# Kernel optimization log

Measured on AMD Instinct MI355X. Metric: run time of the kernel, lower is better.

Reference implementation:

```python
import jax, jax.numpy as jnp
import numpy as np

DEPTH, DIM, HEADS, DIM_HEAD = 6, 1024, 16, 64
INNER = HEADS * DIM_HEAD  # 1024
DFF = 4 * DIM             # 4096
SCALE = DIM_HEAD ** -0.5


def setup_inputs() -> dict:
    key = jax.random.key(0)
    ks = jax.random.split(key, 12)
    def w(k, shape, fan_in):
        return jax.random.normal(k, shape, dtype=jnp.float32) * (fan_in ** -0.5)
    return {
        "x":     jax.random.normal(ks[0], (2, 2048, DIM), dtype=jnp.float32),
        "Wq":    w(ks[1], (DEPTH, DIM, INNER), DIM),
        "Wkv":   w(ks[2], (DEPTH, DIM, 2 * INNER), DIM),
        "Wo":    w(ks[3], (DEPTH, INNER, DIM), INNER),
        "bo":    jnp.zeros((DEPTH, DIM), dtype=jnp.float32),
        "ln1_g": jnp.ones((DEPTH, DIM), dtype=jnp.float32),
        "ln1_b": jnp.zeros((DEPTH, DIM), dtype=jnp.float32),
        "ln2_g": jnp.ones((DEPTH, DIM), dtype=jnp.float32),
        "ln2_b": jnp.zeros((DEPTH, DIM), dtype=jnp.float32),
        "W1":    w(ks[4], (DEPTH, DIM, DFF), DIM),
        "b1":    jnp.zeros((DEPTH, DFF), dtype=jnp.float32),
        "W2":    w(ks[5], (DEPTH, DFF, DIM), DFF),
        "b2":    jnp.zeros((DEPTH, DIM), dtype=jnp.float32),
    }


def _layernorm(x, g, b, eps=1e-5):
    mu = jnp.mean(x, axis=-1, keepdims=True)
    var = jnp.mean(jnp.square(x - mu), axis=-1, keepdims=True)
    return (x - mu) * jax.lax.rsqrt(var + eps) * g + b


def reference(x, Wq, Wkv, Wo, bo, ln1_g, ln1_b, ln2_g, ln2_b, W1, b1, W2, b2):
    b, n, _ = x.shape
    for l in range(DEPTH):
        # --- PreNorm self-attention ---
        h = _layernorm(x, ln1_g[l], ln1_b[l])
        q = h @ Wq[l]                       # [b, n, inner]
        kv = h @ Wkv[l]
        k, v = jnp.split(kv, 2, axis=-1)
        def heads(t):
            return t.reshape(b, n, HEADS, DIM_HEAD).transpose(0, 2, 1, 3)  # [b, h, n, d]
        q, k, v = heads(q), heads(k), heads(v)
        dots = jnp.einsum('bhid,bhjd->bhij', q, k) * SCALE
        attn = jax.nn.softmax(dots, axis=-1)
        out = jnp.einsum('bhij,bhjd->bhid', attn, v)
        out = out.transpose(0, 2, 1, 3).reshape(b, n, INNER)
        x = out @ Wo[l] + bo[l] + x
        # --- PreNorm feed-forward (exact GELU, matching torch nn.GELU default) ---
        h = _layernorm(x, ln2_g[l], ln2_b[l])
        h = jax.nn.gelu(h @ W1[l] + b1[l], approximate=False)
        x = h @ W2[l] + b2[l] + x
    return x
```

## Files before the change

### kernel.cpp

```cpp
#include <hip/hip_runtime.h>
#include <hip/hip_bf16.h>
#include <cstdint>
#include <cstddef>

#define DEPTH 6
#define DIM   1024
#define HEADS 16
#define DIMH  64
#define INNER 1024
#define DFF   4096
#define SEQ   2048
#define NTOK  4096

typedef __attribute__((ext_vector_type(8))) short bf16x8;
typedef __attribute__((ext_vector_type(4))) short bf16x4;
typedef __attribute__((ext_vector_type(4))) float f32x4;
typedef __hip_bfloat16 bf16;

#define CS 0.18033688011112042f
#define SMAX 24.0f

__device__ __forceinline__ void gld_lds16(const void* g, void* l) {
  __builtin_amdgcn_global_load_lds(
      (const __attribute__((address_space(1))) unsigned int*)g,
      (__attribute__((address_space(3))) unsigned int*)l,
      16, 0, 0);
}

__global__ __launch_bounds__(256) void transpose_convert(
    const float* __restrict__ in, bf16* __restrict__ out,
    int K, int N, int row0, int orows)
{
  __shared__ float tile[32][33];
  const int d  = blockIdx.z;
  const int n0 = blockIdx.x * 32, k0 = blockIdx.y * 32;
  const int c = threadIdx.x & 31, rb = threadIdx.x >> 5;
  const float* src = in + ((size_t)d * K + k0) * N + n0;
#pragma unroll
  for (int rr = 0; rr < 4; ++rr) {
    int r = rb + rr * 8;
    tile[r][c] = src[(size_t)r * N + c];
  }
  __syncthreads();
  bf16* dst = out + ((size_t)d * orows + row0 + n0) * K + k0;
#pragma unroll
  for (int rr = 0; rr < 4; ++rr) {
    int r = rb + rr * 8;
    dst[(size_t)r * K + c] = __float2bfloat16(tile[c][r]);
  }
}

__global__ __launch_bounds__(256) void ln_kernel(
    const float* __restrict__ x, const float* __restrict__ g,
    const float* __restrict__ b, bf16* __restrict__ h)
{
  const int row = blockIdx.x;
  const int tid = threadIdx.x;
  const float4 xv = *(const float4*)(x + (size_t)row * DIM + tid * 4);
  float s  = xv.x + xv.y + xv.z + xv.w;
  float s2 = xv.x * xv.x + xv.y * xv.y + xv.z * xv.z + xv.w * xv.w;
#pragma unroll
  for (int off = 1; off < 64; off <<= 1) {
    s  += __shfl_xor(s, off);
    s2 += __shfl_xor(s2, off);
  }
  __shared__ float red[8];
  const int wave = tid >> 6, lane = tid & 63;
  if (lane == 0) { red[wave * 2] = s; red[wave * 2 + 1] = s2; }
  __syncthreads();
  const float ts  = red[0] + red[2] + red[4] + red[6];
  const float ts2 = red[1] + red[3] + red[5] + red[7];
  const float mu  = ts * (1.0f / DIM);
  const float var = ts2 * (1.0f / DIM) - mu * mu;
  const float rstd = rsqrtf(var + 1e-5f);
  const float4 gv = *(const float4*)(g + tid * 4);
  const float4 bv = *(const float4*)(b + tid * 4);
  bf16 hv[4];
  hv[0] = __float2bfloat16((xv.x - mu) * rstd * gv.x + bv.x);
  hv[1] = __float2bfloat16((xv.y - mu) * rstd * gv.y + bv.y);
  hv[2] = __float2bfloat16((xv.z - mu) * rstd * gv.z + bv.z);
  hv[3] = __float2bfloat16((xv.w - mu) * rstd * gv.w + bv.w);
  *(uint2*)(h + (size_t)row * DIM + tid * 4) = *(uint2*)hv;
}

template<int EPI, bool SWZ, int BN>
__global__ __launch_bounds__(256) void gemm_t(
    const bf16* __restrict__ A, const bf16* __restrict__ Bt,
    int N, int K,
    const float* __restrict__ bias,
    float* __restrict__ outf, bf16* __restrict__ outb,
    bf16* __restrict__ outq, bf16* __restrict__ outk, bf16* __restrict__ outvt)
{
  constexpr int NW = BN / 32;
  __shared__ alignas(16) bf16 As[128 * 64];
  __shared__ alignas(16) bf16 Bs[BN * 64];
  const int tid  = threadIdx.x;
  const int lane = tid & 63;
  const int wave = tid >> 6;
  const int wr = wave >> 1, wc = wave & 1;

  int bx, by;
  if (SWZ) {
    const int gx   = (int)gridDim.x;
    const int nwg  = gx * (int)gridDim.y;
    const int wg   = blockIdx.x + blockIdx.y * gx;
    const int xcd  = wg & 7;
    const int slot = wg >> 3;
    const int id   = xcd * (nwg >> 3) + slot;
    by = id / gx;
    bx = id % gx;
  } else {
    bx = blockIdx.x; by = blockIdx.y;
  }
  const int m0 = by * 128, n0 = bx * BN;
  const int sr = tid >> 3, pc = tid & 7;
  const int wbase = (tid & ~63) << 4;

  f32x4 acc[4][NW];
#pragma unroll
  for (int m = 0; m < 4; ++m)
#pragma unroll
    for (int n = 0; n < NW; ++n) acc[m][n] = (f32x4){0.f, 0.f, 0.f, 0.f};

  for (int k0 = 0; k0 < K; k0 += 64) {
#pragma unroll
    for (int it = 0; it < 4; ++it) {
      const int r  = it * 32 + sr;
      const int lc = pc ^ (r & 7);
      gld_lds16(A + (size_t)(m0 + r) * K + k0 + lc * 8, (char*)As + it * 4096 + wbase);
    }
#pragma unroll
    for (int it = 0; it < NW; ++it) {
      const int r  = it * 32 + sr;
      const int lc = pc ^ (r & 7);
      gld_lds16(Bt + (size_t)(n0 + r) * K + k0 + lc * 8, (char*)Bs + it * 4096 + wbase);
    }
    __syncthreads();
#pragma unroll
    for (int kk = 0; kk < 2; ++kk) {
      const int cb = kk * 4 + (lane >> 4);
      bf16x8 af[4], bfr[NW];
#pragma unroll
      for (int m = 0; m < 4; ++m) {
        const int r = wr * 64 + m * 16 + (lane & 15);
        af[m] = *(const bf16x8*)((const char*)As + r * 128 + ((cb ^ (r & 7)) << 4));
      }
#pragma unroll
      for (int n = 0; n < NW; ++n) {
        const int r = wc * (BN / 2) + n * 16 + (lane & 15);
        bfr[n] = *(const bf16x8*)((const char*)Bs + r * 128 + ((cb ^ (r & 7)) << 4));
      }
#pragma unroll
      for (int m = 0; m < 4; ++m)
#pragma unroll
        for (int n = 0; n < NW; ++n)
          acc[m][n] = __builtin_amdgcn_mfma_f32_16x16x32_bf16(af[m], bfr[n], acc[m][n], 0, 0, 0);
    }
    __syncthreads();
  }

#pragma unroll
  for (int m = 0; m < 4; ++m) {
    const int rb = m0 + wr * 64 + m * 16 + ((lane >> 4) << 2);
#pragma unroll
    for (int n = 0; n < NW; ++n) {
      const int col = n0 + wc * (BN / 2) + n * 16 + (lane & 15);
      if (EPI == 0 && col >= 2048) {
        const int batch = rb >> 11, tok = rb & 2047;
        const int c = col - 2048;
        union { bf16x4 v4; short s[4]; } w;
#pragma unroll
        for (int j = 0; j < 4; ++j) {
          const bf16 bb = __float2bfloat16(acc[m][n][j]);
          w.s[j] = *(const short*)&bb;
        }
        *(bf16x4*)(outvt + (((size_t)(batch * HEADS + (c >> 6))) * DIMH + (c & 63)) * SEQ + tok)
            = w.v4;
        continue;
      }
#pragma unroll
      for (int j = 0; j < 4; ++j) {
        const int row = rb + j;
        const float v = acc[m][n][j];
        if (EPI == 0) {
          const int batch = row >> 11, tok = row & 2047;
          if (col < 1024) {
            outq[(((size_t)(batch * HEADS + (col >> 6))) * SEQ + tok) * DIMH + (col & 63)] =
                __float2bfloat16(v * CS);
          } else {
            const int c = col - 1024;
            outk[(((size_t)(batch * HEADS + (c >> 6))) * SEQ + tok) * DIMH + (c & 63)] =
                __float2bfloat16(v);
          }
        } else if (EPI == 1) {
          const size_t off = (size_t)row * N + col;
          outf[off] = v + bias[col] + outf[off];
        } else if (EPI == 2) {
          const float t = v + bias[col];
          const float gg = 0.5f * t * (1.0f + erff(t * 0.70710678118654752f));
          outb[(size_t)row * N + col] = __float2bfloat16(gg);
        }
      }
    }
  }
}

__global__ __launch_bounds__(512) void attn_kernel(
    const bf16* __restrict__ q, const bf16* __restrict__ k,
    const bf16* __restrict__ vt, bf16* __restrict__ out)
{
  __shared__ alignas(16) bf16 Ks[2][2][64 * 64];
  __shared__ alignas(16) bf16 Vs[2][2][64 * 64];
  const int tid  = threadIdx.x;
  const int lane = tid & 63;
  const int wave = tid >> 6;
  const int g    = lane >> 4;
  const int lm   = lane & 15;
  const int bh   = blockIdx.y;
  const int qw   = blockIdx.x * 256 + wave * 32;
  const int sr = tid >> 3, pc = tid & 7;

  bf16x8 qf[2][2];
#pragma unroll
  for (int m = 0; m < 2; ++m)
#pragma unroll
    for (int kk = 0; kk < 2; ++kk)
      qf[m][kk] = *(const bf16x8*)(q + ((size_t)bh * SEQ + qw + m * 16 + lm) * DIMH
                                   + kk * 32 + g * 8);

  f32x4 ao[2][4];
#pragma unroll
  for (int m = 0; m < 2; ++m)
#pragma unroll
    for (int n = 0; n < 4; ++n) ao[m][n] = (f32x4){0.f, 0.f, 0.f, 0.f};
  float lrow[2] = {0.f, 0.f};

  const int lc = pc ^ (sr & 7);
  auto stage = [&](int jt2, int buf) {
#pragma unroll
    for (int sub = 0; sub < 2; ++sub) {
      const int jt = jt2 * 2 + sub;
      gld_lds16(k  + ((size_t)bh * SEQ + jt * 64 + sr) * DIMH + lc * 8,
                (char*)&Ks[buf][sub][0] + tid * 16);
      gld_lds16(vt + ((size_t)bh * DIMH + sr) * SEQ + jt * 64 + lc * 8,
                (char*)&Vs[buf][sub][0] + tid * 16);
    }
  };

  stage(0, 0);

  for (int jt2 = 0; jt2 < SEQ / 128; ++jt2) {
    const int buf = jt2 & 1;
    const bool pref = (jt2 + 1 < SEQ / 128);
    if (pref) {
      stage(jt2 + 1, buf ^ 1);
      asm volatile("s_waitcnt vmcnt(4)" ::: "memory");
    } else {
      asm volatile("s_waitcnt vmcnt(0)" ::: "memory");
    }
    __builtin_amdgcn_s_barrier();

#pragma unroll
    for (int sub = 0; sub < 2; ++sub) {
      f32x4 sa[2][4];
#pragma unroll
      for (int m = 0; m < 2; ++m)
#pragma unroll
        for (int n = 0; n < 4; ++n)
          sa[m][n] = (f32x4){-SMAX, -SMAX, -SMAX, -SMAX};
      __builtin_amdgcn_s_setprio(1);
#pragma unroll
      for (int kk = 0; kk < 2; ++kk)
#pragma unroll
        for (int n = 0; n < 4; ++n) {
          const int row = n * 16 + lm;
          const bf16x8 af = *(const bf16x8*)((const char*)&Ks[buf][sub][0] + row * 128
                                             + (((kk * 4 + g) ^ (row & 7)) << 4));
#pragma unroll
          for (int m = 0; m < 2; ++m)
            sa[m][n] = __builtin_amdgcn_mfma_f32_16x16x32_bf16(af, qf[m][kk], sa[m][n], 0, 0, 0);
        }
      __builtin_amdgcn_s_setprio(0);

      bf16x8 pa[2][2];
#pragma unroll
      for (int m = 0; m < 2; ++m) {
        float rs = 0.f;
#pragma unroll
        for (int n = 0; n < 4; ++n)
#pragma unroll
          for (int r = 0; r < 4; ++r) {
            const float p = exp2f(sa[m][n][r]);
            sa[m][n][r] = p;
            rs += p;
          }
        rs += __shfl_xor(rs, 16);
        rs += __shfl_xor(rs, 32);
        lrow[m] += rs;
#pragma unroll
        for (int h = 0; h < 2; ++h) {
          union { bf16x8 v8; short s[8]; } u;
#pragma unroll
          for (int n2 = 0; n2 < 2; ++n2)
#pragma unroll
            for (int r = 0; r < 4; ++r) {
              const bf16 bb = __float2bfloat16(sa[m][h * 2 + n2][r]);
              u.s[n2 * 4 + r] = *(const short*)&bb;
            }
          pa[m][h] = u.v8;
        }
      }

      __builtin_amdgcn_s_setprio(1);
#pragma unroll
      for (int n = 0; n < 4; ++n) {
        const int row = n * 16 + lm;
        const char* vb = (const char*)&Vs[buf][sub][0] + row * 128;
        const int sw = row & 7;
#pragma unroll
        for (int kk = 0; kk < 2; ++kk) {
          const bf16x4 lo = *(const bf16x4*)(vb + (((kk * 4 + (g >> 1)) ^ sw) << 4) + (g & 1) * 8);
          const bf16x4 hi = *(const bf16x4*)(vb + (((kk * 4 + 2 + (g >> 1)) ^ sw) << 4) + (g & 1) * 8);
          const bf16x8 vf = __builtin_shufflevector(lo, hi, 0, 1, 2, 3, 4, 5, 6, 7);
#pragma unroll
          for (int m = 0; m < 2; ++m)
            ao[m][n] = __builtin_amdgcn_mfma_f32_16x16x32_bf16(vf, pa[m][kk], ao[m][n], 0, 0, 0);
        }
      }
      __builtin_amdgcn_s_setprio(0);
    }
    __builtin_amdgcn_s_barrier();
  }

  const int batch = bh >> 4, head = bh & 15;
#pragma unroll
  for (int m = 0; m < 2; ++m) {
    const float linv = 1.0f / lrow[m];
    const int row = qw + m * 16 + lm;
    bf16* orow = out + ((size_t)batch * SEQ + row) * INNER + head * DIMH;
#pragma unroll
    for (int n = 0; n < 4; ++n) {
      union { bf16x4 v4; short s[4]; } w;
#pragma unroll
      for (int r = 0; r < 4; ++r) {
        const bf16 bb = __float2bfloat16(ao[m][n][r] * linv);
        w.s[r] = *(const short*)&bb;
      }
      *(bf16x4*)(orow + n * 16 + g * 4) = w.v4;
    }
  }
}

extern "C" void kernel_launch(void* const* d_in, const int* in_sizes, int n_in,
                              void* d_out, int out_size, void* d_ws, size_t ws_size,
                              hipStream_t stream)
{
  (void)in_sizes; (void)n_in; (void)out_size; (void)ws_size;
  const float* x_in = (const float*)d_in[0];
  const float* Wq   = (const float*)d_in[1];
  const float* Wkv  = (const float*)d_in[2];
  const float* Wo   = (const float*)d_in[3];
  const float* bo   = (const float*)d_in[4];
  const float* ln1g = (const float*)d_in[5];
  const float* ln1b = (const float*)d_in[6];
  const float* ln2g = (const float*)d_in[7];
  const float* ln2b = (const float*)d_in[8];
  const float* W1   = (const float*)d_in[9];
  const float* b1   = (const float*)d_in[10];
  const float* W2   = (const float*)d_in[11];
  const float* b2   = (const float*)d_in[12];
  float* xb = (float*)d_out;

  char* ws = (char*)d_ws;
  size_t off = 0;
  auto take = [&](size_t bytes) {
    char* p = ws + off;
    off += (bytes + 255) & ~(size_t)255;
    return p;
  };
  bf16* Wqkvt = (bf16*)take((size_t)DEPTH * 3072 * 1024 * 2);
  bf16* Wot   = (bf16*)take((size_t)DEPTH * 1024 * 1024 * 2);
  bf16* W1t   = (bf16*)take((size_t)DEPTH * 4096 * 1024 * 2);
  bf16* W2t   = (bf16*)take((size_t)DEPTH * 1024 * 4096 * 2);
  bf16* hb    = (bf16*)take((size_t)NTOK * DIM * 2);
  bf16* qbuf  = (bf16*)take((size_t)NTOK * INNER * 2);
  bf16* kbuf  = (bf16*)take((size_t)NTOK * INNER * 2);
  bf16* vtbuf = (bf16*)take((size_t)NTOK * INNER * 2);
  bf16* aobuf = (bf16*)take((size_t)NTOK * INNER * 2);
  bf16* h1buf = (bf16*)take((size_t)NTOK * DFF * 2);

  hipMemcpyAsync(xb, x_in, (size_t)NTOK * DIM * 4, hipMemcpyDeviceToDevice, stream);

  dim3 b256(256);
  dim3 b512(512);
  transpose_convert<<<dim3(32, 32, DEPTH),  b256, 0, stream>>>(Wq,  Wqkvt, 1024, 1024, 0,    3072);
  transpose_convert<<<dim3(64, 32, DEPTH),  b256, 0, stream>>>(Wkv, Wqkvt, 1024, 2048, 1024, 3072);
  transpose_convert<<<dim3(32, 32, DEPTH),  b256, 0, stream>>>(Wo,  Wot,   1024, 1024, 0,    1024);
  transpose_convert<<<dim3(128, 32, DEPTH), b256, 0, stream>>>(W1,  W1t,   1024, 4096, 0,    4096);
  transpose_convert<<<dim3(32, 128, DEPTH), b256, 0, stream>>>(W2,  W2t,   4096, 1024, 0,    1024);

  for (int l = 0; l < DEPTH; ++l) {
    ln_kernel<<<NTOK, b256, 0, stream>>>(xb, ln1g + l * DIM, ln1b + l * DIM, hb);
    gemm_t<0, true, 128><<<dim3(3072 / 128, NTOK / 128), b256, 0, stream>>>(
        hb, Wqkvt + (size_t)l * 3072 * 1024, 3072, 1024,
        nullptr, nullptr, nullptr, qbuf, kbuf, vtbuf);
    attn_kernel<<<dim3(SEQ / 256, 32), b512, 0, stream>>>(qbuf, kbuf, vtbuf, aobuf);
    gemm_t<1, true, 64><<<dim3(1024 / 64, NTOK / 128), b256, 0, stream>>>(
        aobuf, Wot + (size_t)l * 1024 * 1024, 1024, 1024,
        bo + l * DIM, xb, nullptr, nullptr, nullptr, nullptr);
    ln_kernel<<<NTOK, b256, 0, stream>>>(xb, ln2g + l * DIM, ln2b + l * DIM, hb);
    gemm_t<2, true, 128><<<dim3(4096 / 128, NTOK / 128), b256, 0, stream>>>(
        hb, W1t + (size_t)l * 4096 * 1024, 4096, 1024,
        b1 + l * DFF, nullptr, h1buf, nullptr, nullptr, nullptr);
    gemm_t<1, true, 64><<<dim3(1024 / 64, NTOK / 128), b256, 0, stream>>>(
        h1buf, W2t + (size_t)l * 1024 * 4096, 1024, 4096,
        b2 + l * DIM, xb, nullptr, nullptr, nullptr, nullptr);
  }
}
```

Baseline: 1.686 ms.

## Use 8-wave GEMM blocks and compute attention row sums with MFMA

The GEMM kernel now launches with 512 threads (8 waves, arranged 4x2 over the 128xBN tile), so each wave owns 32 rows instead of 64. Per-wave accumulators and loads are halved, and the launch bound asks for 4 blocks per CU, aiming at more waves in flight to hide latency. In the attention kernel, the scalar exp-sum plus cross-lane shuffle reduction is replaced by an extra MFMA that multiplies a ones vector by the bf16 probabilities. That moves the row-sum work onto the matrix units, at the cost of summing bf16-rounded probabilities and issuing extra MFMAs.

```diff
diff --git a/kernel.cpp b/kernel.cpp
--- a/kernel.cpp
+++ b/kernel.cpp
@@ -84,7 +84,7 @@
 }
 
 template<int EPI, bool SWZ, int BN>
-__global__ __launch_bounds__(256) void gemm_t(
+__global__ __launch_bounds__(512, 4) void gemm_t(
     const bf16* __restrict__ A, const bf16* __restrict__ Bt,
     int N, int K,
     const float* __restrict__ bias,
@@ -92,12 +92,14 @@
     bf16* __restrict__ outq, bf16* __restrict__ outk, bf16* __restrict__ outvt)
 {
   constexpr int NW = BN / 32;
+  constexpr int NB = BN / 64;
   __shared__ alignas(16) bf16 As[128 * 64];
   __shared__ alignas(16) bf16 Bs[BN * 64];
   const int tid  = threadIdx.x;
   const int lane = tid & 63;
   const int wave = tid >> 6;
-  const int wr = wave >> 1, wc = wave & 1;
+  const int wr = wave >> 1;
+  const int wc = wave & 1;
 
   int bx, by;
   if (SWZ) {
@@ -115,34 +117,31 @@
   const int m0 = by * 128, n0 = bx * BN;
   const int sr = tid >> 3, pc = tid & 7;
   const int wbase = (tid & ~63) << 4;
-
-  f32x4 acc[4][NW];
-#pragma unroll
-  for (int m = 0; m < 4; ++m)
+  const int lc = pc ^ (sr & 7);
+
+  f32x4 acc[2][NW];
+#pragma unroll
+  for (int m = 0; m < 2; ++m)
 #pragma unroll
     for (int n = 0; n < NW; ++n) acc[m][n] = (f32x4){0.f, 0.f, 0.f, 0.f};
 
   for (int k0 = 0; k0 < K; k0 += 64) {
 #pragma unroll
-    for (int it = 0; it < 4; ++it) {
-      const int r  = it * 32 + sr;
-      const int lc = pc ^ (r & 7);
-      gld_lds16(A + (size_t)(m0 + r) * K + k0 + lc * 8, (char*)As + it * 4096 + wbase);
-    }
-#pragma unroll
-    for (int it = 0; it < NW; ++it) {
-      const int r  = it * 32 + sr;
-      const int lc = pc ^ (r & 7);
-      gld_lds16(Bt + (size_t)(n0 + r) * K + k0 + lc * 8, (char*)Bs + it * 4096 + wbase);
-    }
+    for (int it = 0; it < 2; ++it)
+      gld_lds16(A + (size_t)(m0 + it * 64 + sr) * K + k0 + lc * 8,
+                (char*)As + it * 8192 + wbase);
+#pragma unroll
+    for (int it = 0; it < NB; ++it)
+      gld_lds16(Bt + (size_t)(n0 + it * 64 + sr) * K + k0 + lc * 8,
+                (char*)Bs + it * 8192 + wbase);
     __syncthreads();
 #pragma unroll
     for (int kk = 0; kk < 2; ++kk) {
       const int cb = kk * 4 + (lane >> 4);
-      bf16x8 af[4], bfr[NW];
-#pragma unroll
-      for (int m = 0; m < 4; ++m) {
-        const int r = wr * 64 + m * 16 + (lane & 15);
+      bf16x8 af[2], bfr[NW];
+#pragma unroll
+      for (int m = 0; m < 2; ++m) {
+        const int r = wr * 32 + m * 16 + (lane & 15);
         af[m] = *(const bf16x8*)((const char*)As + r * 128 + ((cb ^ (r & 7)) << 4));
       }
 #pragma unroll
@@ -151,7 +150,7 @@
         bfr[n] = *(const bf16x8*)((const char*)Bs + r * 128 + ((cb ^ (r & 7)) << 4));
       }
 #pragma unroll
-      for (int m = 0; m < 4; ++m)
+      for (int m = 0; m < 2; ++m)
 #pragma unroll
         for (int n = 0; n < NW; ++n)
           acc[m][n] = __builtin_amdgcn_mfma_f32_16x16x32_bf16(af[m], bfr[n], acc[m][n], 0, 0, 0);
@@ -160,8 +159,8 @@
   }
 
 #pragma unroll
-  for (int m = 0; m < 4; ++m) {
-    const int rb = m0 + wr * 64 + m * 16 + ((lane >> 4) << 2);
+  for (int m = 0; m < 2; ++m) {
+    const int rb = m0 + wr * 32 + m * 16 + ((lane >> 4) << 2);
 #pragma unroll
     for (int n = 0; n < NW; ++n) {
       const int col = n0 + wc * (BN / 2) + n * 16 + (lane & 15);
@@ -228,12 +227,17 @@
       qf[m][kk] = *(const bf16x8*)(q + ((size_t)bh * SEQ + qw + m * 16 + lm) * DIMH
                                    + kk * 32 + g * 8);
 
+  union { bf16x8 v8; short s[8]; } ones_u;
+#pragma unroll
+  for (int i = 0; i < 8; ++i) ones_u.s[i] = 0x3F80;
+  const bf16x8 onesA = ones_u.v8;
+
   f32x4 ao[2][4];
 #pragma unroll
   for (int m = 0; m < 2; ++m)
 #pragma unroll
     for (int n = 0; n < 4; ++n) ao[m][n] = (f32x4){0.f, 0.f, 0.f, 0.f};
-  float lrow[2] = {0.f, 0.f};
+  f32x4 lsum[2] = {(f32x4){0.f, 0.f, 0.f, 0.f}, (f32x4){0.f, 0.f, 0.f, 0.f}};
 
   const int lc = pc ^ (sr & 7);
   auto stage = [&](int jt2, int buf) {
@@ -285,18 +289,11 @@
       bf16x8 pa[2][2];
 #pragma unroll
       for (int m = 0; m < 2; ++m) {
-        float rs = 0.f;
 #pragma unroll
         for (int n = 0; n < 4; ++n)
 #pragma unroll
-          for (int r = 0; r < 4; ++r) {
-            const float p = exp2f(sa[m][n][r]);
-            sa[m][n][r] = p;
-            rs += p;
-          }
-        rs += __shfl_xor(rs, 16);
-        rs += __shfl_xor(rs, 32);
-        lrow[m] += rs;
+          for (int r = 0; r < 4; ++r)
+            sa[m][n][r] = exp2f(sa[m][n][r]);
 #pragma unroll
         for (int h = 0; h < 2; ++h) {
           union { bf16x8 v8; short s[8]; } u;
@@ -313,6 +310,11 @@
 
       __builtin_amdgcn_s_setprio(1);
 #pragma unroll
+      for (int m = 0; m < 2; ++m)
+#pragma unroll
+        for (int kk = 0; kk < 2; ++kk)
+          lsum[m] = __builtin_amdgcn_mfma_f32_16x16x32_bf16(onesA, pa[m][kk], lsum[m], 0, 0, 0);
+#pragma unroll
       for (int n = 0; n < 4; ++n) {
         const int row = n * 16 + lm;
         const char* vb = (const char*)&Vs[buf][sub][0] + row * 128;
@@ -335,7 +337,7 @@
   const int batch = bh >> 4, head = bh & 15;
 #pragma unroll
   for (int m = 0; m < 2; ++m) {
-    const float linv = 1.0f / lrow[m];
+    const float linv = 1.0f / lsum[m][0];
     const int row = qw + m * 16 + lm;
     bf16* orow = out + ((size_t)batch * SEQ + row) * INNER + head * DIMH;
 #pragma unroll
@@ -401,18 +403,18 @@
 
   for (int l = 0; l < DEPTH; ++l) {
     ln_kernel<<<NTOK, b256, 0, stream>>>(xb, ln1g + l * DIM, ln1b + l * DIM, hb);
-    gemm_t<0, true, 128><<<dim3(3072 / 128, NTOK / 128), b256, 0, stream>>>(
+    gemm_t<0, true, 128><<<dim3(3072 / 128, NTOK / 128), b512, 0, stream>>>(
         hb, Wqkvt + (size_t)l * 3072 * 1024, 3072, 1024,
         nullptr, nullptr, nullptr, qbuf, kbuf, vtbuf);
     attn_kernel<<<dim3(SEQ / 256, 32), b512, 0, stream>>>(qbuf, kbuf, vtbuf, aobuf);
-    gemm_t<1, true, 64><<<dim3(1024 / 64, NTOK / 128), b256, 0, stream>>>(
+    gemm_t<1, true, 64><<<dim3(1024 / 64, NTOK / 128), b512, 0, stream>>>(
         aobuf, Wot + (size_t)l * 1024 * 1024, 1024, 1024,
         bo + l * DIM, xb, nullptr, nullptr, nullptr, nullptr);
     ln_kernel<<<NTOK, b256, 0, stream>>>(xb, ln2g + l * DIM, ln2b + l * DIM, hb);
-    gemm_t<2, true, 128><<<dim3(4096 / 128, NTOK / 128), b256, 0, stream>>>(
+    gemm_t<2, true, 128><<<dim3(4096 / 128, NTOK / 128), b512, 0, stream>>>(
         hb, W1t + (size_t)l * 4096 * 1024, 4096, 1024,
         b1 + l * DFF, nullptr, h1buf, nullptr, nullptr, nullptr);
-    gemm_t<1, true, 64><<<dim3(1024 / 64, NTOK / 128), b256, 0, stream>>>(
+    gemm_t<1, true, 64><<<dim3(1024 / 64, NTOK / 128), b512, 0, stream>>>(
         h1buf, W2t + (size_t)l * 1024 * 4096, 1024, 4096,
         b2 + l * DIM, xb, nullptr, nullptr, nullptr, nullptr);
   }
```

Result: faster. 1.532 ms (-9.2%).
